# Kernel tuning notes

Measured on AMD Instinct MI355X. Metric: run time of the kernel, lower is better.

Reference implementation:

```python
import math
import jax, jax.numpy as jnp
from jax import lax
import numpy as np

NUM_HEADS = 8

def conv2d(x, w, b):
    # x: [N,C,H,W], w: [O,I,3,3], padding=1 == SAME
    y = lax.conv_general_dilated(x, w, (1, 1), 'SAME',
                                 dimension_numbers=('NCHW', 'OIHW', 'NCHW'))
    return y + b[None, :, None, None]

def setup_inputs() -> dict:
    key = jax.random.key(0)
    ks = jax.random.split(key, 10)
    B, L, C = 64, 196, 768
    K, R = 8192, 8
    return {
        'in_feas': jax.random.normal(ks[0], (B, L, C), jnp.float32),
        'cur_f': 4,
        'codebook': jax.random.normal(ks[1], (K, C), jnp.float32),
        'att_w': jax.random.normal(ks[2], (R, C, 3, 3), jnp.float32) * 0.02,
        'att_b': jnp.zeros((R,), jnp.float32),
        'ex_w': jax.random.normal(ks[3], (1, C, 3, 3), jnp.float32) * 0.02,
        'ex_b': jnp.zeros((1,), jnp.float32),
        'qkv_w': jax.random.normal(ks[4], (3 * C, C), jnp.float32) * 0.02,
        'qkv_b': jnp.zeros((3 * C,), jnp.float32),
        'proj_w': jax.random.normal(ks[5], (C, C), jnp.float32) * 0.02,
        'proj_b': jnp.zeros((C,), jnp.float32),
    }

def attention(x, qkv_w, qkv_b, proj_w, proj_b):
    # x: [B, N, C], standard multi-head self-attention
    B, N, C = x.shape
    dh = C // NUM_HEADS
    qkv = x @ qkv_w.T + qkv_b                          # [B,N,3C]
    qkv = qkv.reshape(B, N, 3, NUM_HEADS, dh).transpose(2, 0, 3, 1, 4)
    q, k, v = qkv[0], qkv[1], qkv[2]                   # [B,H,N,dh]
    attn = jax.nn.softmax(jnp.einsum('bhnd,bhmd->bhnm', q, k) * (dh ** -0.5), axis=-1)
    out = jnp.einsum('bhnm,bhmd->bhnd', attn, v)
    out = out.transpose(0, 2, 1, 3).reshape(B, N, C)
    return out @ proj_w.T + proj_b

def reference(in_feas, cur_f, codebook, att_w, att_b, ex_w, ex_b,
              qkv_w, qkv_b, proj_w, proj_b):
    B, L, C = in_feas.shape
    h = int(math.sqrt(L)); w = L // h
    R = att_w.shape[0]

    # ---- Vector quantization: cdist + argmin + codebook gather ----
    flat = in_feas.reshape(-1, C)                      # [B*L, C]
    d = (jnp.sum(flat * flat, axis=1, keepdims=True)
         - 2.0 * flat @ codebook.T
         + jnp.sum(codebook * codebook, axis=1)[None, :])   # [B*L, K]
    idx = jnp.argmin(d, axis=1)                        # [B*L]
    quant = codebook[idx]                              # gather
    vq = flat + lax.stop_gradient(quant - flat)        # straight-through
    enc = idx.reshape(-1, h, w)                        # [B, h, w]

    # ---- Motion excitation (cur_f > 1) ----
    Bp = B // cur_f
    x = in_feas.reshape(Bp, cur_f, L, C)
    diff = x - jnp.concatenate([x[:, :1], x[:, :-1]], axis=1)  # frame diff, first frame zero
    dmap = diff.reshape(-1, L, C).transpose(0, 2, 1).reshape(-1, C, h, w)
    mm = conv2d(dmap, ex_w, ex_b).reshape(Bp, cur_f, L)
    mm = jax.nn.softmax(mm, axis=-1)
    motion = (x * mm[..., None]).reshape(-1, C)
    vq = vq + motion

    # ---- Aggregation: region attention conv + masked pooling (as one einsum) ----
    xm = vq.reshape(B, L, C).transpose(0, 2, 1).reshape(B, C, h, w)
    region_mask = conv2d(xm, att_w, att_b)             # [B,R,h,w]
    regions = jnp.einsum('bchw,brhw->bcr', xm, region_mask) / (h * w)  # [B,C,R]
    vd = regions.transpose(0, 2, 1)                    # [B,R,C]

    # ---- Interaction: self-attention over T*S region tokens ----
    seq = vd.reshape(Bp, cur_f * R, C)
    seq = attention(seq, qkv_w, qkv_b, proj_w, proj_b)
    vd = seq.reshape(-1, R, C)                         # [B,R,C]
    return (vd, enc, region_mask)
```

## Files before the change

### kernel.cpp

```cpp
#include <hip/hip_runtime.h>
#include <math.h>

#define B_   64
#define L_   196
#define C_   768
#define K_   8192
#define R_   8
#define HW_  14
#define M_   (B_*L_)
#define NH_  8
#define DH_  96
#define BP_  16
#define NT_  32

typedef unsigned short ushort_t;
typedef __attribute__((ext_vector_type(8))) short short8v;
typedef __attribute__((ext_vector_type(4))) float f32x4;
typedef __attribute__((ext_vector_type(4))) int   i32x4;

__device__ inline float wave_reduce_sum(float v) {
    #pragma unroll
    for (int o = 32; o >= 1; o >>= 1) v += __shfl_xor(v, o, 64);
    return v;
}
__device__ inline float wave_reduce_max(float v) {
    #pragma unroll
    for (int o = 32; o >= 1; o >>= 1) v = fmaxf(v, __shfl_xor(v, o, 64));
    return v;
}

__device__ inline ushort_t f2bf_rne(float f) {
    unsigned u = __float_as_uint(f);
    unsigned r = u + 0x7fffu + ((u >> 16) & 1u);
    return (ushort_t)(r >> 16);
}
__device__ inline float bf2f(ushort_t h) { return __uint_as_float(((unsigned)h) << 16); }

__device__ inline char q8(float f, float s) {
    int q = __float2int_rn(f * s);
    return (char)(q < -127 ? -127 : (q > 127 ? 127 : q));
}

__device__ inline void gload_lds16(const void* gsrc, void* ldst) {
    __builtin_amdgcn_global_load_lds(
        (const __attribute__((address_space(1))) unsigned int*)gsrc,
        (__attribute__((address_space(3))) unsigned int*)ldst, 16, 0, 0);
}

__device__ inline void top2_merge(float& v1, int& i1, float& v2, int& i2,
                                  float w1, int j1, float w2, int j2) {
    bool fw = (v1 < w1) || (v1 == w1 && i1 <= j1);
    float a1 = fw ? v1 : w1;  int ai1 = fw ? i1 : j1;
    float lb = fw ? w1 : v1;  int lbi = fw ? j1 : i1;
    float wsv = fw ? v2 : w2; int wsi = fw ? i2 : j2;
    bool sb = (lb < wsv) || (lb == wsv && lbi < wsi);
    v1 = a1; i1 = ai1;
    v2 = sb ? lb : wsv; i2 = sb ? lbi : wsi;
}

__device__ inline void ce4(float& v0, int& j0, float& v1, int& j1) {
    bool sw = (v1 < v0) || (v1 == v0 && j1 < j0);
    float tv = sw ? v1 : v0, uv = sw ? v0 : v1;
    int tj = sw ? j1 : j0, uj = sw ? j0 : j1;
    v0 = tv; j0 = tj; v1 = uv; j1 = uj;
}
__device__ inline void pickmin(float& v, int& j, float bv, int bj) {
    if (bv < v || (bv == v && bj < j)) { v = bv; j = bj; }
}

__global__ __launch_bounds__(256) void cbq_kernel(const float* __restrict__ CB,
                                                  char* __restrict__ CBq,
                                                  float* __restrict__ cnq) {
    __shared__ float xs[16 * 776];
    const int t = threadIdx.x;
    const int blk = blockIdx.x;
    const float4* src = (const float4*)(CB + (size_t)blk * 16 * C_);
    #pragma unroll
    for (int i = 0; i < 12; ++i) {
        int idx4 = t + i * 256;
        int r = idx4 / 192, c4 = idx4 - r * 192;
        ((float4*)(xs + r * 776))[c4] = src[idx4];
    }
    __syncthreads();
    #pragma unroll
    for (int i = 0; i < 3; ++i) {
        int s = t + i * 256;
        int kb = s >> 6, l = s & 63;
        int row = l & 15;
        int k0 = kb * 64 + ((l >> 4) << 4);
        union { char c[16]; i32x4 v; } Q;
        #pragma unroll
        for (int e = 0; e < 16; ++e) Q.c[e] = q8(xs[row * 776 + k0 + e], 32.f);
        *(i32x4*)&CBq[(((size_t)blk * 12 + kb) << 10) + l * 16] = Q.v;
    }
    int row = t & 15, chunk = t >> 4;
    float sum = 0.f;
    #pragma unroll
    for (int j = 0; j < 48; ++j) { float v = xs[row * 776 + chunk * 48 + j]; sum += v * v; }
    sum += __shfl_xor(sum, 16, 64);
    sum += __shfl_xor(sum, 32, 64);
    __shared__ float red[4][16];
    if ((t & 63) < 16) red[t >> 6][t & 15] = sum;
    __syncthreads();
    if (t < 16) cnq[blk * 16 + t] = (red[0][t] + red[1][t] + red[2][t] + red[3][t]) * 1024.f;
}

__global__ __launch_bounds__(256) void aq_kernel(const float* __restrict__ X,
                                                 char* __restrict__ Aq) {
    __shared__ float xs[16 * 776];
    const int t = threadIdx.x;
    const int rg = blockIdx.x;
    const float4* src = (const float4*)(X + (size_t)rg * 16 * C_);
    #pragma unroll
    for (int i = 0; i < 12; ++i) {
        int idx4 = t + i * 256;
        int r = idx4 / 192, c4 = idx4 - r * 192;
        ((float4*)(xs + r * 776))[c4] = src[idx4];
    }
    __syncthreads();
    #pragma unroll
    for (int i = 0; i < 3; ++i) {
        int s = t + i * 256;
        int kb = s >> 6, l = s & 63;
        int row = l & 15;
        int k0 = kb * 64 + ((l >> 4) << 4);
        union { char c[16]; i32x4 v; } Q;
        #pragma unroll
        for (int e = 0; e < 16; ++e) Q.c[e] = q8(xs[row * 776 + k0 + e], 32.f);
        *(i32x4*)&Aq[(((size_t)rg * 12 + kb) << 10) + l * 16] = Q.v;
    }
}

__global__ __launch_bounds__(256) void wsplit_kernel(const float* __restrict__ att_w,
                                                     const float* __restrict__ ex_w,
                                                     ushort_t* __restrict__ attHi,
                                                     char* __restrict__ exq) {
    int gid = blockIdx.x * 256 + threadIdx.x;
    if (gid < 7680) {
        int cb = gid / 1536;
        int rem = gid - cb * 1536;
        int l = rem & 63;
        int col = cb * 16 + (l & 15);
        int k = ((rem >> 6) << 5) + ((l >> 4) << 3);
        union { ushort_t u[8]; short8v v; } H;
        #pragma unroll
        for (int e = 0; e < 8; ++e) {
            int c = k + e;
            float f = (col < 72) ? att_w[(size_t)(col & 7) * 6912 + c * 9 + (col >> 3)] : 0.f;
            H.u[e] = f2bf_rne(f);
        }
        *(short8v*)&attHi[(size_t)gid * 8] = H.v;
    } else if (gid < 8448) {
        int g2 = gid - 7680;
        int l = g2 & 63;
        int col = l & 15;
        int k0 = ((g2 >> 6) << 6) + ((l >> 4) << 4);
        union { char c[16]; i32x4 v; } Q;
        #pragma unroll
        for (int e = 0; e < 16; ++e) {
            int k = k0 + e;
            float f = (col < 9) ? ex_w[k * 9 + col] : 0.f;
            Q.c[e] = q8(f, 1024.f);
        }
        *(i32x4*)&exq[(size_t)g2 * 16] = Q.v;
    }
}

__global__ __launch_bounds__(256) void wgemm_split_kernel(const float* __restrict__ qkv_w,
                                                          const float* __restrict__ proj_w,
                                                          ushort_t* __restrict__ wqkvF,
                                                          ushort_t* __restrict__ wprojF) {
    int gid = blockIdx.x * 256 + threadIdx.x;
    const float* W; ushort_t* D; int g2;
    if (gid < 221184) { W = qkv_w; D = wqkvF; g2 = gid; }
    else { W = proj_w; D = wprojF; g2 = gid - 221184; }
    int cb = g2 / 1536;
    int rem = g2 - cb * 1536;
    int l = rem & 63;
    int col = cb * 16 + (l & 15);
    int k = ((rem >> 6) << 5) + ((l >> 4) << 3);
    union { ushort_t u[8]; short8v v; } H;
    #pragma unroll
    for (int e = 0; e < 8; ++e) H.u[e] = f2bf_rne(W[(size_t)col * 768 + k + e]);
    *(short8v*)&D[(size_t)g2 * 8] = H.v;
}

__global__ __launch_bounds__(256, 2) void vq_i8_kernel(const char* __restrict__ Aq,
                                                       const char* __restrict__ CBq,
                                                       const float* __restrict__ cnq,
                                                       float4* __restrict__ cand) {
    __shared__ __align__(16) char AqL[2][4096];
    __shared__ __align__(16) char BqL[2][32768];
    const int tid = threadIdx.x;
    const int l = tid & 63, w = tid >> 6;
    const int g = blockIdx.x;
    const int mt = blockIdx.y;
    const int row0 = mt * 64;
    const int rg0 = mt * 4;

    float v1[4][4], v2[4][4]; int i1[4][4], i2[4][4];
    #pragma unroll
    for (int mf = 0; mf < 4; ++mf)
        #pragma unroll
        for (int rg = 0; rg < 4; ++rg) {
            v1[mf][rg] = INFINITY; v2[mf][rg] = INFINITY;
            i1[mf][rg] = 0x7fffffff; i2[mf][rg] = 0x7fffffff;
        }

    auto STAGE = [&](int buf, int u) {
        int ch = (u >= 12) ? 1 : 0;
        int st = u - ch * 12;
        int cbase = g * 64 + ch * 32;
        #pragma unroll
        for (int i = 0; i < 9; ++i) {
            int s = w * 9 + i;
            if (s < 4)
                gload_lds16(&Aq[(((size_t)(rg0 + s) * 12 + st) << 10) + l * 16],
                            &AqL[buf][s << 10]);
            else {
                int cb = s - 4;
                gload_lds16(&CBq[(((size_t)(cbase + cb) * 12 + st) << 10) + l * 16],
                            &BqL[buf][cb << 10]);
            }
        }
    };

    int cur = 0;
    STAGE(0, 0);
    __syncthreads();

    #pragma unroll 1
    for (int ch = 0; ch < 2; ++ch) {
        i32x4 acc[4][8];
        #pragma unroll
        for (int mf = 0; mf < 4; ++mf)
            #pragma unroll
            for (int nf = 0; nf < 8; ++nf) acc[mf][nf] = (i32x4){0, 0, 0, 0};

        #pragma unroll 1
        for (int st = 0; st < 12; ++st) {
            int u = ch * 12 + st;
            if (u < 23) STAGE(cur ^ 1, u + 1);
            i32x4 aq[4];
            #pragma unroll
            for (int mf = 0; mf < 4; ++mf)
                aq[mf] = *(const i32x4*)&AqL[cur][(mf << 10) + l * 16];
            #pragma unroll
            for (int nf = 0; nf < 8; ++nf) {
                i32x4 bq = *(const i32x4*)&BqL[cur][((w * 8 + nf) << 10) + l * 16];
                #pragma unroll
                for (int mf = 0; mf < 4; ++mf)
                    acc[mf][nf] = __builtin_amdgcn_mfma_i32_16x16x64_i8(aq[mf], bq, acc[mf][nf], 0, 0, 0);
            }
            asm volatile("s_waitcnt vmcnt(9)" ::: "memory");
            __builtin_amdgcn_sched_barrier(0);
            __builtin_amdgcn_s_barrier();
            __builtin_amdgcn_sched_barrier(0);
            cur ^= 1;
        }
        #pragma unroll
        for (int nf = 0; nf < 8; ++nf) {
            int code = g * 1024 + ch * 512 + w * 128 + nf * 16 + (l & 15);
            float cnv = cnq[code];
            #pragma unroll
            for (int mf = 0; mf < 4; ++mf)
                #pragma unroll
                for (int rg = 0; rg < 4; ++rg) {
                    float d = fmaf(-2.f, (float)acc[mf][nf][rg], cnv);
                    bool c1 = d < v1[mf][rg];
                    bool c2 = d < v2[mf][rg];
                    float nv2 = c1 ? v1[mf][rg] : (c2 ? d : v2[mf][rg]);
                    int   ni2 = c1 ? i1[mf][rg] : (c2 ? code : i2[mf][rg]);
                    v2[mf][rg] = nv2; i2[mf][rg] = ni2;
                    if (c1) { v1[mf][rg] = d; i1[mf][rg] = code; }
                }
        }
    }
    #pragma unroll
    for (int mf = 0; mf < 4; ++mf)
        #pragma unroll
        for (int rg = 0; rg < 4; ++rg) {
            float a1 = v1[mf][rg], a2 = v2[mf][rg];
            int b1 = i1[mf][rg], b2 = i2[mf][rg];
            #pragma unroll
            for (int off = 8; off >= 1; off >>= 1) {
                float w1 = __shfl_xor(a1, off, 64), w2 = __shfl_xor(a2, off, 64);
                int j1 = __shfl_xor(b1, off, 64), j2 = __shfl_xor(b2, off, 64);
                top2_merge(a1, b1, a2, b2, w1, j1, w2, j2);
            }
            if ((l & 15) == 0) {
                int row = row0 + mf * 16 + (l >> 4) * 4 + rg;
                cand[(size_t)row * 32 + g * 4 + w] =
                    make_float4(a1, __int_as_float(b1), a2, __int_as_float(b2));
            }
        }
}

__global__ __launch_bounds__(256) void rescore_kernel(const float4* __restrict__ cand,
                                                      const float* __restrict__ X,
                                                      const float* __restrict__ CB,
                                                      int* __restrict__ idx,
                                                      float* __restrict__ encOut) {
    int w = threadIdx.x >> 6, l = threadIdx.x & 63;
    int r = blockIdx.x * 4 + w;
    float a0, a1, a2, a3; int j0, j1, j2, j3;
    if (l < 32) {
        float4 c = cand[(size_t)r * 32 + l];
        a0 = c.x; j0 = __float_as_int(c.y);
        a1 = c.z; j1 = __float_as_int(c.w);
    } else { a0 = INFINITY; a1 = INFINITY; j0 = 0x7fffffff; j1 = 0x7fffffff; }
    a2 = INFINITY; a3 = INFINITY; j2 = 0x7fffffff; j3 = 0x7fffffff;
    #pragma unroll
    for (int off = 32; off >= 1; off >>= 1) {
        float b0 = __shfl_xor(a0, off, 64), b1 = __shfl_xor(a1, off, 64);
        float b2 = __shfl_xor(a2, off, 64), b3 = __shfl_xor(a3, off, 64);
        int p0 = __shfl_xor(j0, off, 64), p1 = __shfl_xor(j1, off, 64);
        int p2 = __shfl_xor(j2, off, 64), p3 = __shfl_xor(j3, off, 64);
        pickmin(a0, j0, b3, p3); pickmin(a1, j1, b2, p2);
        pickmin(a2, j2, b1, p1); pickmin(a3, j3, b0, p0);
        ce4(a0, j0, a2, j2); ce4(a1, j1, a3, j3);
        ce4(a0, j0, a1, j1); ce4(a2, j2, a3, j3);
    }
    double dot0 = 0, dot1 = 0, dot2 = 0, dot3 = 0;
    double nn0 = 0, nn1 = 0, nn2 = 0, nn3 = 0;
    const float* xr = X + (size_t)r * C_;
    #pragma unroll
    for (int jj = 0; jj < 12; ++jj) {
        int c = l * 12 + jj;
        double x = (double)xr[c];
        double c0 = (double)CB[(size_t)j0 * C_ + c]; dot0 += x * c0; nn0 += c0 * c0;
        double c1 = (double)CB[(size_t)j1 * C_ + c]; dot1 += x * c1; nn1 += c1 * c1;
        double c2 = (double)CB[(size_t)j2 * C_ + c]; dot2 += x * c2; nn2 += c2 * c2;
        double c3 = (double)CB[(size_t)j3 * C_ + c]; dot3 += x * c3; nn3 += c3 * c3;
    }
    #pragma unroll
    for (int off = 32; off >= 1; off >>= 1) {
        dot0 += __shfl_xor(dot0, off, 64); dot1 += __shfl_xor(dot1, off, 64);
        dot2 += __shfl_xor(dot2, off, 64); dot3 += __shfl_xor(dot3, off, 64);
        nn0 += __shfl_xor(nn0, off, 64); nn1 += __shfl_xor(nn1, off, 64);
        nn2 += __shfl_xor(nn2, off, 64); nn3 += __shfl_xor(nn3, off, 64);
    }
    if (l == 0) {
        double d0 = nn0 - 2.0 * dot0, d1 = nn1 - 2.0 * dot1;
        double d2 = nn2 - 2.0 * dot2, d3 = nn3 - 2.0 * dot3;
        double best = d0; int bi = j0;
        if (d1 < best || (d1 == best && j1 < bi)) { best = d1; bi = j1; }
        if (d2 < best || (d2 == best && j2 < bi)) { best = d2; bi = j2; }
        if (d3 < best || (d3 == best && j3 < bi)) { best = d3; bi = j3; }
        idx[r] = bi;
        encOut[r] = (float)bi;
    }
}

__global__ __launch_bounds__(256) void convgemm_i8_kernel(const char* __restrict__ Aq,
                                                          const char* __restrict__ Bq,
                                                          float* __restrict__ out) {
    __shared__ __align__(16) char AqL[8 * 1024];
    __shared__ __align__(16) char BqL[1024];
    const int tid = threadIdx.x;
    const int l = tid & 63, w = tid >> 6;
    const int rg0 = blockIdx.x * 8, row0 = blockIdx.x * 128;
    i32x4 acc[2];
    acc[0] = (i32x4){0, 0, 0, 0}; acc[1] = (i32x4){0, 0, 0, 0};
    #pragma unroll 1
    for (int st = 0; st < 12; ++st) {
        __syncthreads();
        #pragma unroll
        for (int i = 0; i < 3; ++i) {
            int s = w * 3 + i;
            if (s < 8)
                gload_lds16(&Aq[(((size_t)(rg0 + s) * 12 + st) << 10) + l * 16], &AqL[s << 10]);
            else if (s == 8)
                gload_lds16(&Bq[((size_t)st << 10) + l * 16], &BqL[0]);
        }
        __syncthreads();
        i32x4 bq = *(const i32x4*)&BqL[l * 16];
        #pragma unroll
        for (int mf = 0; mf < 2; ++mf) {
            i32x4 aq = *(const i32x4*)&AqL[((w * 2 + mf) << 10) + l * 16];
            acc[mf] = __builtin_amdgcn_mfma_i32_16x16x64_i8(aq, bq, acc[mf], 0, 0, 0);
        }
    }
    #pragma unroll
    for (int mf = 0; mf < 2; ++mf)
        #pragma unroll
        for (int rg = 0; rg < 4; ++rg) {
            int row = row0 + w * 32 + mf * 16 + (l >> 4) * 4 + rg;
            out[(size_t)row * 16 + (l & 15)] = (float)acc[mf][rg] * (1.f / 32768.f);
        }
}

template<int NF>
__global__ __launch_bounds__(256) void convgemm_kernel(const ushort_t* __restrict__ Ahi_g,
                                                       const ushort_t* __restrict__ Bhi_g,
                                                       float* __restrict__ out) {
    __shared__ __align__(16) ushort_t AhL[16 * 512];
    __shared__ __align__(16) ushort_t BhL[NF * 2 * 512];
    const int TOT = 16 + 2 * NF;
    const int PW = (TOT + 3) >> 2;
    const int tid = threadIdx.x;
    const int l = tid & 63, w = tid >> 6;
    const int rg0 = blockIdx.x * 8;
    const int row0 = blockIdx.x * 128;
    f32x4 acc[2][NF];
    #pragma unroll
    for (int mf = 0; mf < 2; ++mf)
        #pragma unroll
        for (int nf = 0; nf < NF; ++nf) acc[mf][nf] = (f32x4){0.f, 0.f, 0.f, 0.f};
    #pragma unroll 1
    for (int st = 0; st < 12; ++st) {
        __syncthreads();
        #pragma unroll
        for (int i = 0; i < PW; ++i) {
            int s = w * PW + i;
            if (s < 16) {
                int rb = s >> 1, kb = s & 1;
                gload_lds16(&Ahi_g[(((size_t)(rg0 + rb) * 24 + st * 2 + kb) << 9) + l * 8], &AhL[s << 9]);
            } else if (s < TOT) {
                int t2 = s - 16;
                int cb = t2 >> 1, kb = t2 & 1;
                gload_lds16(&Bhi_g[(((size_t)cb * 24 + st * 2 + kb) << 9) + l * 8], &BhL[t2 << 9]);
            }
        }
        __syncthreads();
        #pragma unroll
        for (int kf = 0; kf < 2; ++kf) {
            short8v ah[2];
            #pragma unroll
            for (int mf = 0; mf < 2; ++mf)
                ah[mf] = *(const short8v*)&AhL[(((w * 2 + mf) * 2 + kf) << 9) + l * 8];
            #pragma unroll
            for (int nf = 0; nf < NF; ++nf) {
                short8v bh = *(const short8v*)&BhL[((nf * 2 + kf) << 9) + l * 8];
                #pragma unroll
                for (int mf = 0; mf < 2; ++mf)
                    acc[mf][nf] = __builtin_amdgcn_mfma_f32_16x16x32_bf16(ah[mf], bh, acc[mf][nf], 0, 0, 0);
            }
        }
    }
    #pragma unroll
    for (int mf = 0; mf < 2; ++mf)
        #pragma unroll
        for (int nf = 0; nf < NF; ++nf)
            #pragma unroll
            for (int rg = 0; rg < 4; ++rg) {
                int row = row0 + w * 32 + mf * 16 + (l >> 4) * 4 + rg;
                out[(size_t)row * (NF * 16) + nf * 16 + (l & 15)] = acc[mf][nf][rg];
            }
}

template<int NF>
__global__ __launch_bounds__(256) void gemm_frag_kernel(const ushort_t* __restrict__ Af,
                                                        const ushort_t* __restrict__ Bf,
                                                        const float* __restrict__ bias,
                                                        float* __restrict__ out, int N) {
    __shared__ __align__(16) ushort_t AhL[16 * 512];
    __shared__ __align__(16) ushort_t BhL[2 * NF * 512];
    const int TOT = 16 + 2 * NF;
    const int PW = (TOT + 3) >> 2;
    const int tid = threadIdx.x;
    const int l = tid & 63, w = tid >> 6;
    const int rg0 = blockIdx.x * 8, row0 = blockIdx.x * 128;
    const int cb0 = blockIdx.y * NF;
    f32x4 acc[2][NF];
    #pragma unroll
    for (int mf = 0; mf < 2; ++mf)
        #pragma unroll
        for (int nf = 0; nf < NF; ++nf) acc[mf][nf] = (f32x4){0.f, 0.f, 0.f, 0.f};
    #pragma unroll 1
    for (int st = 0; st < 12; ++st) {
        __syncthreads();
        #pragma unroll
        for (int i = 0; i < PW; ++i) {
            int s = w * PW + i;
            if (s < 16) {
                int rb = s >> 1, kb = s & 1;
                gload_lds16(&Af[(((size_t)(rg0 + rb) * 24 + st * 2 + kb) << 9) + l * 8], &AhL[s << 9]);
            } else if (s < TOT) {
                int t2 = s - 16;
                int cb = t2 >> 1, kb = t2 & 1;
                gload_lds16(&Bf[(((size_t)(cb0 + cb) * 24 + st * 2 + kb) << 9) + l * 8], &BhL[t2 << 9]);
            }
        }
        __syncthreads();
        #pragma unroll
        for (int kf = 0; kf < 2; ++kf) {
            short8v ah[2];
            #pragma unroll
            for (int mf = 0; mf < 2; ++mf)
                ah[mf] = *(const short8v*)&AhL[(((w * 2 + mf) * 2 + kf) << 9) + l * 8];
            #pragma unroll
            for (int nf = 0; nf < NF; ++nf) {
                short8v bh = *(const short8v*)&BhL[((nf * 2 + kf) << 9) + l * 8];
                #pragma unroll
                for (int mf = 0; mf < 2; ++mf)
                    acc[mf][nf] = __builtin_amdgcn_mfma_f32_16x16x32_bf16(ah[mf], bh, acc[mf][nf], 0, 0, 0);
            }
        }
    }
    #pragma unroll
    for (int mf = 0; mf < 2; ++mf)
        #pragma unroll
        for (int nf = 0; nf < NF; ++nf) {
            int col = (cb0 + nf) * 16 + (l & 15);
            float bv = bias[col];
            #pragma unroll
            for (int rg = 0; rg < 4; ++rg) {
                int row = row0 + w * 32 + mf * 16 + (l >> 4) * 4 + rg;
                out[(size_t)row * N + col] = acc[mf][nf][rg] + bv;
            }
        }
}

__global__ __launch_bounds__(256) void mm_finish_kernel(const float* __restrict__ XW,
                                                        const float* __restrict__ ex_b,
                                                        float* __restrict__ sm) {
    int b = blockIdx.x, t = threadIdx.x;
    float val = -INFINITY;
    if (t < L_) {
        if ((b & 3) == 0) val = ex_b[0];
        else {
            int yy = t / HW_, xx = t - (t / HW_) * HW_;
            float acc = 0.f;
            #pragma unroll
            for (int dy = 0; dy < 3; ++dy) {
                int sy = yy + dy - 1; if (sy < 0 || sy >= HW_) continue;
                #pragma unroll
                for (int dx = 0; dx < 3; ++dx) {
                    int sx = xx + dx - 1; if (sx < 0 || sx >= HW_) continue;
                    int q = sy * HW_ + sx, tap = dy * 3 + dx;
                    acc += XW[((size_t)b * L_ + q) * 16 + tap]
                         - XW[((size_t)(b - 1) * L_ + q) * 16 + tap];
                }
            }
            val = acc + ex_b[0];
        }
    }
    __shared__ float red[4];
    float mw = wave_reduce_max(val);
    if ((t & 63) == 0) red[t >> 6] = mw;
    __syncthreads();
    float mx = fmaxf(fmaxf(red[0], red[1]), fmaxf(red[2], red[3]));
    float e = (t < L_) ? expf(val - mx) : 0.f;
    __syncthreads();
    float sw = wave_reduce_sum(e);
    if ((t & 63) == 0) red[t >> 6] = sw;
    __syncthreads();
    float s = red[0] + red[1] + red[2] + red[3];
    if (t < L_) sm[b * L_ + t] = e / s;
}

__global__ __launch_bounds__(256) void vqf_split_kernel(const float* __restrict__ X,
                                                        const float* __restrict__ CB,
                                                        const int* __restrict__ idx,
                                                        const float* __restrict__ sm,
                                                        ushort_t* __restrict__ Vhi) {
    const int rg = blockIdx.x, t = threadIdx.x;
    #pragma unroll
    for (int i = 0; i < 6; ++i) {
        int s = t + i * 256;
        int kb = s >> 6, l = s & 63;
        int row = rg * 16 + (l & 15);
        int k = kb * 32 + ((l >> 4) << 3);
        int kidx = idx[row];
        float sc = sm[row];
        const float* xp = &X[(size_t)row * C_ + k];
        const float* cp = &CB[(size_t)kidx * C_ + k];
        union { ushort_t u[8]; short8v v; } H;
        #pragma unroll
        for (int e = 0; e < 8; ++e) H.u[e] = f2bf_rne(cp[e] + xp[e] * sc);
        *(short8v*)&Vhi[((size_t)rg * 1536 + s) * 8] = H.v;
    }
}

__global__ __launch_bounds__(256) void rm_finish_kernel(const float* __restrict__ OUTC,
                                                        const float* __restrict__ att_b,
                                                        float* __restrict__ rmOut) {
    int gid = blockIdx.x * 256 + threadIdx.x;
    if (gid >= B_ * R_ * L_) return;
    int b = gid / (R_ * L_);
    int rem = gid - b * (R_ * L_);
    int r = rem / L_, p = rem - r * L_;
    int yy = p / HW_, xx = p - yy * HW_;
    float acc = att_b[r];
    #pragma unroll
    for (int dy = 0; dy < 3; ++dy) {
        int sy = yy + dy - 1; if (sy < 0 || sy >= HW_) continue;
        #pragma unroll
        for (int dx = 0; dx < 3; ++dx) {
            int sx = xx + dx - 1; if (sx < 0 || sx >= HW_) continue;
            int q = sy * HW_ + sx, tap = dy * 3 + dx;
            acc += OUTC[((size_t)b * L_ + q) * 80 + tap * 8 + r];
        }
    }
    rmOut[gid] = acc;
}

__global__ __launch_bounds__(256) void regions_kernel(const ushort_t* __restrict__ Vhi,
                                                      const float* __restrict__ rm,
                                                      ushort_t* __restrict__ seqF) {
    int b = blockIdx.x, cg = blockIdx.y, t = threadIdx.x;
    __shared__ float rms[R_ * L_];
    for (int i = t; i < R_ * L_; i += 256) rms[i] = rm[(size_t)b * R_ * L_ + i];
    __syncthreads();
    const float inv = 1.f / 196.f;
    int c = cg * 256 + t;
    int kb = c >> 5, q = (c >> 3) & 3, e = c & 7;
    float acc[R_] = {};
    for (int p = 0; p < L_; ++p) {
        int row = b * L_ + p;
        int rg = row >> 4, rr = row & 15;
        size_t a = (((size_t)rg * 24 + kb) * 64 + q * 16 + rr) * 8 + e;
        float x = bf2f(Vhi[a]);
        #pragma unroll
        for (int r = 0; r < R_; ++r) acc[r] += x * rms[r * L_ + p];
    }
    #pragma unroll
    for (int r = 0; r < R_; ++r) {
        int row = b * 8 + r;
        int rg2 = row >> 4, rr = row & 15;
        seqF[(((size_t)rg2 * 24 + kb) * 64 + q * 16 + rr) * 8 + e] = f2bf_rne(acc[r] * inv);
    }
}

__global__ __launch_bounds__(256) void attn_kernel(const float* __restrict__ qkv,
                                                   ushort_t* __restrict__ outF) {
    int bp = blockIdx.x, h = blockIdx.y;
    __shared__ float qs[NT_][DH_], ks[NT_][DH_], vs[NT_][DH_];
    __shared__ float sc[NT_][NT_ + 1];
    int tid = threadIdx.x;
    for (int e = tid; e < NT_ * DH_; e += 256) {
        int n = e / DH_, d = e - n * DH_;
        size_t base = ((size_t)(bp * NT_ + n)) * 2304 + h * DH_ + d;
        qs[n][d] = qkv[base];
        ks[n][d] = qkv[base + 768];
        vs[n][d] = qkv[base + 1536];
    }
    __syncthreads();
    const float scale = 1.0f / sqrtf((float)DH_);
    for (int e = tid; e < NT_ * NT_; e += 256) {
        int n = e >> 5, m = e & 31;
        float s = 0.f;
        #pragma unroll 8
        for (int d = 0; d < DH_; ++d) s += qs[n][d] * ks[m][d];
        sc[n][m] = s * scale;
    }
    __syncthreads();
    if (tid < NT_) {
        float mx = -INFINITY;
        #pragma unroll
        for (int m = 0; m < NT_; ++m) mx = fmaxf(mx, sc[tid][m]);
        float sum = 0.f;
        #pragma unroll
        for (int m = 0; m < NT_; ++m) { float e2 = expf(sc[tid][m] - mx); sc[tid][m] = e2; sum += e2; }
        float inv = 1.f / sum;
        #pragma unroll
        for (int m = 0; m < NT_; ++m) sc[tid][m] *= inv;
    }
    __syncthreads();
    for (int e = tid; e < NT_ * DH_; e += 256) {
        int n = e / DH_, d = e - n * DH_;
        float o = 0.f;
        #pragma unroll
        for (int m = 0; m < NT_; ++m) o += sc[n][m] * vs[m][d];
        int row = bp * NT_ + n, c = h * DH_ + d;
        outF[(((size_t)(row >> 4) * 24 + (c >> 5)) * 64 + ((c >> 3) & 3) * 16 + (row & 15)) * 8 + (c & 7)]
            = f2bf_rne(o);
    }
}

extern "C" void kernel_launch(void* const* d_in, const int* in_sizes, int n_in,
                              void* d_out, int out_size, void* d_ws, size_t ws_size,
                              hipStream_t stream) {
    const float* in_feas  = (const float*)d_in[0];
    const float* codebook = (const float*)d_in[2];
    const float* att_w    = (const float*)d_in[3];
    const float* att_b    = (const float*)d_in[4];
    const float* ex_w     = (const float*)d_in[5];
    const float* ex_b     = (const float*)d_in[6];
    const float* qkv_w    = (const float*)d_in[7];
    const float* qkv_b    = (const float*)d_in[8];
    const float* proj_w   = (const float*)d_in[9];
    const float* proj_b   = (const float*)d_in[10];

    float* out    = (float*)d_out;
    float* outVd  = out;
    float* outEnc = out + 393216;
    float* outRm  = out + 393216 + 12544;

    float* ws = (float*)d_ws;
    float*    cnq    = ws + 0;
    float4*   cand   = (float4*)(ws + 8192);
    char*     CBq    = (char*)(ws + 1613824);
    char*     Aq     = (char*)(ws + 3186688);
    ushort_t* attHi  = (ushort_t*)(ws + 5595136);
    char*     exq    = (char*)(ws + 5625856);
    ushort_t* wqkvF  = (ushort_t*)(ws + 5628928);
    ushort_t* wprojF = (ushort_t*)(ws + 6513664);
    int*      idx    = (int*)(ws + 6808576);
    float*    XW     = ws + 6821120;
    float*    sm     = ws + 7021824;
    ushort_t* Vhi    = (ushort_t*)(ws + 7034368);
    float*    OUTC   = ws + 11851264;
    ushort_t* seqF   = (ushort_t*)(ws + 12854784);
    float*    qkvb   = ws + 13051392;
    ushort_t* attnbF = (ushort_t*)(ws + 14231040);

    hipLaunchKernelGGL(cbq_kernel, dim3(512), dim3(256), 0, stream, codebook, CBq, cnq);
    hipLaunchKernelGGL(aq_kernel, dim3(784), dim3(256), 0, stream, in_feas, Aq);
    hipLaunchKernelGGL(wsplit_kernel, dim3(33), dim3(256), 0, stream, att_w, ex_w, attHi, exq);
    hipLaunchKernelGGL(wgemm_split_kernel, dim3(1152), dim3(256), 0, stream,
                       qkv_w, proj_w, wqkvF, wprojF);
    hipLaunchKernelGGL(vq_i8_kernel, dim3(8, 196), dim3(256), 0, stream, Aq, CBq, cnq, cand);
    hipLaunchKernelGGL(convgemm_i8_kernel, dim3(98), dim3(256), 0, stream, Aq, exq, XW);
    hipLaunchKernelGGL(rescore_kernel, dim3(M_ / 4), dim3(256), 0, stream,
                       cand, in_feas, codebook, idx, outEnc);
    hipLaunchKernelGGL(mm_finish_kernel, dim3(B_), dim3(256), 0, stream, XW, ex_b, sm);
    hipLaunchKernelGGL(vqf_split_kernel, dim3(784), dim3(256), 0, stream,
                       in_feas, codebook, idx, sm, Vhi);
    hipLaunchKernelGGL((convgemm_kernel<5>), dim3(98), dim3(256), 0, stream, Vhi, attHi, OUTC);
    hipLaunchKernelGGL(rm_finish_kernel, dim3(392), dim3(256), 0, stream, OUTC, att_b, outRm);
    hipLaunchKernelGGL(regions_kernel, dim3(B_, 3), dim3(256), 0, stream, Vhi, outRm, seqF);
    hipLaunchKernelGGL((gemm_frag_kernel<8>), dim3(4, 18), dim3(256), 0, stream,
                       seqF, wqkvF, qkv_b, qkvb, 2304);
    hipLaunchKernelGGL(attn_kernel, dim3(BP_, NH_), dim3(256), 0, stream, qkvb, attnbF);
    hipLaunchKernelGGL((gemm_frag_kernel<8>), dim3(4, 6), dim3(256), 0, stream,
                       attnbF, wprojF, proj_b, outVd, 768);
}
```

Baseline: 345.0 us.

## Pack codebook indices into low mantissa bits of distances for min/max top-2 selection

The int8 VQ distance kernel now keeps its top-2 candidates by overwriting the low mantissa bits of each distance with a local code tag. This lets plain fminf/fmaxf replace the compare-and-select logic on separate value/index registers, and halves the candidate buffer from float4 to float2. The rescore kernel splices the lane id into the tag and decodes the full code index from the winning value. Other changes precompute the staging address offsets, hoist the codebook-norm loads before the loop, and raise wave priority around the MFMA block. Truncating mantissa bits slightly perturbs distances and tie ordering, but rescoring the top-4 candidates in double precision should hide that.

```diff
diff --git a/kernel.cpp b/kernel.cpp
--- a/kernel.cpp
+++ b/kernel.cpp
@@ -18,6 +18,8 @@
 typedef __attribute__((ext_vector_type(4))) float f32x4;
 typedef __attribute__((ext_vector_type(4))) int   i32x4;
 
+#define BIGF __uint_as_float(0x7F000000u)
+
 __device__ inline float wave_reduce_sum(float v) {
     #pragma unroll
     for (int o = 32; o >= 1; o >>= 1) v += __shfl_xor(v, o, 64);
@@ -45,27 +47,6 @@
     __builtin_amdgcn_global_load_lds(
         (const __attribute__((address_space(1))) unsigned int*)gsrc,
         (__attribute__((address_space(3))) unsigned int*)ldst, 16, 0, 0);
-}
-
-__device__ inline void top2_merge(float& v1, int& i1, float& v2, int& i2,
-                                  float w1, int j1, float w2, int j2) {
-    bool fw = (v1 < w1) || (v1 == w1 && i1 <= j1);
-    float a1 = fw ? v1 : w1;  int ai1 = fw ? i1 : j1;
-    float lb = fw ? w1 : v1;  int lbi = fw ? j1 : i1;
-    float wsv = fw ? v2 : w2; int wsi = fw ? i2 : j2;
-    bool sb = (lb < wsv) || (lb == wsv && lbi < wsi);
-    v1 = a1; i1 = ai1;
-    v2 = sb ? lb : wsv; i2 = sb ? lbi : wsi;
-}
-
-__device__ inline void ce4(float& v0, int& j0, float& v1, int& j1) {
-    bool sw = (v1 < v0) || (v1 == v0 && j1 < j0);
-    float tv = sw ? v1 : v0, uv = sw ? v0 : v1;
-    int tj = sw ? j1 : j0, uj = sw ? j0 : j1;
-    v0 = tv; j0 = tj; v1 = uv; j1 = uj;
-}
-__device__ inline void pickmin(float& v, int& j, float bv, int bj) {
-    if (bv < v || (bv == v && bj < j)) { v = bv; j = bj; }
 }
 
 __global__ __launch_bounds__(256) void cbq_kernel(const float* __restrict__ CB,
@@ -188,7 +169,7 @@
 __global__ __launch_bounds__(256, 2) void vq_i8_kernel(const char* __restrict__ Aq,
                                                        const char* __restrict__ CBq,
                                                        const float* __restrict__ cnq,
-                                                       float4* __restrict__ cand) {
+                                                       float2* __restrict__ cand) {
     __shared__ __align__(16) char AqL[2][4096];
     __shared__ __align__(16) char BqL[2][32768];
     const int tid = threadIdx.x;
@@ -198,36 +179,40 @@
     const int row0 = mt * 64;
     const int rg0 = mt * 4;
 
-    float v1[4][4], v2[4][4]; int i1[4][4], i2[4][4];
+    int K[9];
+    #pragma unroll
+    for (int i = 0; i < 9; ++i) {
+        int s = w * 9 + i;
+        K[i] = ((s < 4) ? (rg0 + s) * 12288 : (g * 64 + (s - 4)) * 12288) + l * 16;
+    }
+    float cnr[2][8];
+    #pragma unroll
+    for (int ch = 0; ch < 2; ++ch)
+        #pragma unroll
+        for (int nf = 0; nf < 8; ++nf)
+            cnr[ch][nf] = cnq[g * 1024 + ch * 512 + w * 128 + nf * 16 + (l & 15)];
+
+    float v1[4][4], v2[4][4];
     #pragma unroll
     for (int mf = 0; mf < 4; ++mf)
         #pragma unroll
-        for (int rg = 0; rg < 4; ++rg) {
-            v1[mf][rg] = INFINITY; v2[mf][rg] = INFINITY;
-            i1[mf][rg] = 0x7fffffff; i2[mf][rg] = 0x7fffffff;
-        }
-
-    auto STAGE = [&](int buf, int u) {
-        int ch = (u >= 12) ? 1 : 0;
-        int st = u - ch * 12;
-        int cbase = g * 64 + ch * 32;
+        for (int rg = 0; rg < 4; ++rg) { v1[mf][rg] = BIGF; v2[mf][rg] = BIGF; }
+
+    auto STAGE = [&](int buf, int oA, int oB) {
         #pragma unroll
         for (int i = 0; i < 9; ++i) {
             int s = w * 9 + i;
             if (s < 4)
-                gload_lds16(&Aq[(((size_t)(rg0 + s) * 12 + st) << 10) + l * 16],
-                            &AqL[buf][s << 10]);
-            else {
-                int cb = s - 4;
-                gload_lds16(&CBq[(((size_t)(cbase + cb) * 12 + st) << 10) + l * 16],
-                            &BqL[buf][cb << 10]);
-            }
+                gload_lds16((const char*)Aq + (unsigned)(K[i] + oA), &AqL[buf][s << 10]);
+            else
+                gload_lds16((const char*)CBq + (unsigned)(K[i] + oB), &BqL[buf][(s - 4) << 10]);
         }
     };
 
     int cur = 0;
-    STAGE(0, 0);
-    __syncthreads();
+    STAGE(0, 0, 0);
+    __syncthreads();
+    int sA = 1024, sB = 1024;
 
     #pragma unroll 1
     for (int ch = 0; ch < 2; ++ch) {
@@ -240,18 +225,27 @@
         #pragma unroll 1
         for (int st = 0; st < 12; ++st) {
             int u = ch * 12 + st;
-            if (u < 23) STAGE(cur ^ 1, u + 1);
+            if (u < 23) {
+                STAGE(cur ^ 1, sA, sB);
+                bool wrap = (((u + 1) % 12) == 11);
+                sA += wrap ? -11264 : 1024;
+                sB += wrap ? 381952 : 1024;
+            }
+            const char* aB = &AqL[cur][l * 16];
+            const char* bB = &BqL[cur][(w * 8) * 1024 + l * 16];
             i32x4 aq[4];
             #pragma unroll
             for (int mf = 0; mf < 4; ++mf)
-                aq[mf] = *(const i32x4*)&AqL[cur][(mf << 10) + l * 16];
+                aq[mf] = *(const i32x4*)(aB + (mf << 10));
+            __builtin_amdgcn_s_setprio(1);
             #pragma unroll
             for (int nf = 0; nf < 8; ++nf) {
-                i32x4 bq = *(const i32x4*)&BqL[cur][((w * 8 + nf) << 10) + l * 16];
+                i32x4 bq = *(const i32x4*)(bB + (nf << 10));
                 #pragma unroll
                 for (int mf = 0; mf < 4; ++mf)
                     acc[mf][nf] = __builtin_amdgcn_mfma_i32_16x16x64_i8(aq[mf], bq, acc[mf][nf], 0, 0, 0);
             }
+            __builtin_amdgcn_s_setprio(0);
             asm volatile("s_waitcnt vmcnt(9)" ::: "memory");
             __builtin_amdgcn_sched_barrier(0);
             __builtin_amdgcn_s_barrier();
@@ -260,19 +254,17 @@
         }
         #pragma unroll
         for (int nf = 0; nf < 8; ++nf) {
-            int code = g * 1024 + ch * 512 + w * 128 + nf * 16 + (l & 15);
-            float cnv = cnq[code];
+            float cnv = cnr[ch][nf];
+            unsigned tag = ((unsigned)ch << 7) | ((unsigned)nf << 4) | (unsigned)(l & 15);
             #pragma unroll
             for (int mf = 0; mf < 4; ++mf)
                 #pragma unroll
                 for (int rg = 0; rg < 4; ++rg) {
                     float d = fmaf(-2.f, (float)acc[mf][nf][rg], cnv);
-                    bool c1 = d < v1[mf][rg];
-                    bool c2 = d < v2[mf][rg];
-                    float nv2 = c1 ? v1[mf][rg] : (c2 ? d : v2[mf][rg]);
-                    int   ni2 = c1 ? i1[mf][rg] : (c2 ? code : i2[mf][rg]);
-                    v2[mf][rg] = nv2; i2[mf][rg] = ni2;
-                    if (c1) { v1[mf][rg] = d; i1[mf][rg] = code; }
+                    float dp = __uint_as_float((__float_as_uint(d) & 0xFFFFFF00u) | tag);
+                    float t = fmaxf(v1[mf][rg], dp);
+                    v1[mf][rg] = fminf(v1[mf][rg], dp);
+                    v2[mf][rg] = fminf(v2[mf][rg], t);
                 }
         }
     }
@@ -281,46 +273,58 @@
         #pragma unroll
         for (int rg = 0; rg < 4; ++rg) {
             float a1 = v1[mf][rg], a2 = v2[mf][rg];
-            int b1 = i1[mf][rg], b2 = i2[mf][rg];
             #pragma unroll
             for (int off = 8; off >= 1; off >>= 1) {
-                float w1 = __shfl_xor(a1, off, 64), w2 = __shfl_xor(a2, off, 64);
-                int j1 = __shfl_xor(b1, off, 64), j2 = __shfl_xor(b2, off, 64);
-                top2_merge(a1, b1, a2, b2, w1, j1, w2, j2);
+                float b1 = __shfl_xor(a1, off, 64), b2 = __shfl_xor(a2, off, 64);
+                float m1 = fminf(a1, b1);
+                float t  = fmaxf(a1, b1);
+                a2 = fminf(t, fminf(a2, b2));
+                a1 = m1;
             }
             if ((l & 15) == 0) {
                 int row = row0 + mf * 16 + (l >> 4) * 4 + rg;
-                cand[(size_t)row * 32 + g * 4 + w] =
-                    make_float4(a1, __int_as_float(b1), a2, __int_as_float(b2));
-            }
-        }
-}
-
-__global__ __launch_bounds__(256) void rescore_kernel(const float4* __restrict__ cand,
+                cand[(size_t)row * 32 + g * 4 + w] = make_float2(a1, a2);
+            }
+        }
+}
+
+__global__ __launch_bounds__(256) void rescore_kernel(const float2* __restrict__ cand,
                                                       const float* __restrict__ X,
                                                       const float* __restrict__ CB,
                                                       int* __restrict__ idx,
                                                       float* __restrict__ encOut) {
     int w = threadIdx.x >> 6, l = threadIdx.x & 63;
     int r = blockIdx.x * 4 + w;
-    float a0, a1, a2, a3; int j0, j1, j2, j3;
+    float a0, a1, a2, a3;
     if (l < 32) {
-        float4 c = cand[(size_t)r * 32 + l];
-        a0 = c.x; j0 = __float_as_int(c.y);
-        a1 = c.z; j1 = __float_as_int(c.w);
-    } else { a0 = INFINITY; a1 = INFINITY; j0 = 0x7fffffff; j1 = 0x7fffffff; }
-    a2 = INFINITY; a3 = INFINITY; j2 = 0x7fffffff; j3 = 0x7fffffff;
+        float2 c = cand[(size_t)r * 32 + l];
+        unsigned b0 = __float_as_uint(c.x), b1 = __float_as_uint(c.y);
+        a0 = __uint_as_float((b0 & 0xFFFFE000u) | ((unsigned)l << 8) | (b0 & 0xFFu));
+        a1 = __uint_as_float((b1 & 0xFFFFE000u) | ((unsigned)l << 8) | (b1 & 0xFFu));
+    } else { a0 = BIGF; a1 = BIGF; }
+    a2 = BIGF; a3 = BIGF;
     #pragma unroll
     for (int off = 32; off >= 1; off >>= 1) {
         float b0 = __shfl_xor(a0, off, 64), b1 = __shfl_xor(a1, off, 64);
         float b2 = __shfl_xor(a2, off, 64), b3 = __shfl_xor(a3, off, 64);
-        int p0 = __shfl_xor(j0, off, 64), p1 = __shfl_xor(j1, off, 64);
-        int p2 = __shfl_xor(j2, off, 64), p3 = __shfl_xor(j3, off, 64);
-        pickmin(a0, j0, b3, p3); pickmin(a1, j1, b2, p2);
-        pickmin(a2, j2, b1, p1); pickmin(a3, j3, b0, p0);
-        ce4(a0, j0, a2, j2); ce4(a1, j1, a3, j3);
-        ce4(a0, j0, a1, j1); ce4(a2, j2, a3, j3);
-    }
+        a0 = fminf(a0, b3); a1 = fminf(a1, b2);
+        a2 = fminf(a2, b1); a3 = fminf(a3, b0);
+        float lo, hi;
+        lo = fminf(a0, a2); hi = fmaxf(a0, a2); a0 = lo; a2 = hi;
+        lo = fminf(a1, a3); hi = fmaxf(a1, a3); a1 = lo; a3 = hi;
+        lo = fminf(a0, a1); hi = fmaxf(a0, a1); a0 = lo; a1 = hi;
+        lo = fminf(a2, a3); hi = fmaxf(a2, a3); a2 = lo; a3 = hi;
+    }
+    int jc[4];
+    float av[4] = {a0, a1, a2, a3};
+    #pragma unroll
+    for (int k = 0; k < 4; ++k) {
+        unsigned bits = __float_as_uint(av[k]);
+        int s = (bits >> 8) & 31;
+        jc[k] = (s >> 2) * 1024 + (int)((bits >> 7) & 1) * 512 + (s & 3) * 128
+              + (int)((bits >> 4) & 7) * 16 + (int)(bits & 15);
+    }
+    int j0 = jc[0], j1 = jc[1], j2 = jc[2], j3 = jc[3];
     double dot0 = 0, dot1 = 0, dot2 = 0, dot3 = 0;
     double nn0 = 0, nn1 = 0, nn2 = 0, nn3 = 0;
     const float* xr = X + (size_t)r * C_;
@@ -690,7 +694,7 @@
 
     float* ws = (float*)d_ws;
     float*    cnq    = ws + 0;
-    float4*   cand   = (float4*)(ws + 8192);
+    float2*   cand   = (float2*)(ws + 8192);
     char*     CBq    = (char*)(ws + 1613824);
     char*     Aq     = (char*)(ws + 3186688);
     ushort_t* attHi  = (ushort_t*)(ws + 5595136);
```

Measured after the change: 312.6 us. 1.1x faster.
